# Optimization experiments

Measured on AMD Instinct MI355X. Metric: run time of the kernel, lower is better.

The kernel has to match this reference:

```python
import jax, jax.numpy as jnp
import numpy as np

N = 50000        # nodes
R = 51           # enriched relations (25 fwd + 25 inverse + self-loop)
F_IN = 32        # feat_size
E = 32           # embed_size
C = 16           # num_classes
B = 30           # num_bases
NNZ = 2_000_000  # nonzeros in vertical adjacency


def _xavier(key, shape):
    # mimics nn.init.xavier_uniform_ with gain for relu (sqrt(2))
    fan_in, fan_out = shape[-2], shape[-1]
    a = np.sqrt(2.0) * np.sqrt(6.0 / (fan_in + fan_out))
    return jax.random.uniform(key, shape, jnp.float32, -a, a)


def setup_inputs() -> dict:
    key = jax.random.key(0)
    ks = jax.random.split(key, 8)
    # COO of vertical adjacency, shape (R*N, N)
    rows = jax.random.randint(ks[0], (NNZ,), 0, R * N)
    cols = jax.random.randint(ks[1], (NNZ,), 0, N)
    # row-normalized values: vals = 1 / row_degree  (sum_sparse with rows=True)
    deg = jax.ops.segment_sum(jnp.ones((NNZ,), jnp.float32), rows, num_segments=R * N)
    vals = (1.0 / jnp.maximum(deg, 1.0))[rows]
    features = jax.random.normal(ks[2], (N, F_IN), jnp.float32)
    comps1 = _xavier(ks[3], (R, B))
    bases1 = _xavier(ks[4], (B, F_IN, E))
    comps2 = _xavier(ks[5], (R, B))
    bases2 = _xavier(ks[6], (B, E, C))
    bias1 = jnp.zeros((E,), jnp.float32)
    bias2 = jnp.zeros((C,), jnp.float32)
    return {
        "features": features, "vals": vals,
        "comps1": comps1, "bases1": bases1, "bias1": bias1,
        "comps2": comps2, "bases2": bases2, "bias2": bias2,
        "rows": rows, "cols": cols,
    }


def _spmm(rows, cols, vals, x):
    # (R*N, N) sparse @ (N, f) dense -> (R*N, f)
    return jax.ops.segment_sum(vals[:, None] * x[cols], rows, num_segments=R * N)


def reference(features, vals, comps1, bases1, bias1, comps2, bases2, bias2, rows, cols):
    # layer 1: SpMM then basis-decomposed per-relation mixing
    h = _spmm(rows, cols, vals, features).reshape(R, N, F_IN)   # (r, n, f)
    w1 = jnp.einsum('rb,bfe->rfe', comps1, bases1)              # (r, f, e)
    h = jnp.einsum('rnf,rfe->ne', h, w1)                        # (n, e)
    h = jax.nn.relu(h + bias1)
    # layer 2
    h = _spmm(rows, cols, vals, h).reshape(R, N, E)             # (r, n, e)
    w2 = jnp.einsum('rb,bho->rho', comps2, bases2)              # (r, e, c)
    h = jnp.einsum('rho,rnh->no', w2, h)                        # (n, c)
    return h + bias2
```

## Files before the change

kernel.cpp:

```cpp
#include <hip/hip_runtime.h>

#define NNODES 50000
#define RREL 51
#define FIN 32
#define EDIM 32
#define CDIM 16
#define BB 30
#define NNZ_ 2000000
#define CAP_ 2000896
#define EPB 4096
#define NBUK 391

typedef unsigned int uint32;
typedef unsigned short ushort;
typedef uint32 u32x2 __attribute__((ext_vector_type(2)));
typedef uint32 u32x4 __attribute__((ext_vector_type(4)));
typedef short bf16x8 __attribute__((ext_vector_type(8)));
typedef float f32x4 __attribute__((ext_vector_type(4)));

static __device__ __forceinline__ uint32 pack_bf16x2(float a, float b) {
    uint32 ua = __builtin_bit_cast(uint32, a);
    uint32 ub = __builtin_bit_cast(uint32, b);
    ua += 0x7fffu + ((ua >> 16) & 1u);
    ub += 0x7fffu + ((ub >> 16) & 1u);
    return (ua >> 16) | (ub & 0xffff0000u);
}
static __device__ __forceinline__ ushort bf16_1(float x) {
    uint32 u = __builtin_bit_cast(uint32, x);
    u += 0x7fffu + ((u >> 16) & 1u);
    return (ushort)(u >> 16);
}
static __device__ __forceinline__ float unpack_lo(uint32 u) { return __builtin_bit_cast(float, u << 16); }
static __device__ __forceinline__ float unpack_hi(uint32 u) { return __builtin_bit_cast(float, u & 0xffff0000u); }

__global__ void k_weights(const float* __restrict__ comps1, const float* __restrict__ bases1,
                          const float* __restrict__ comps2, const float* __restrict__ bases2,
                          ushort* __restrict__ Wb1, ushort* __restrict__ Wb2) {
    int i = blockIdx.x * 256 + threadIdx.x;
    if (i < RREL * FIN * EDIM) {
        int r = i >> 10, fe = i & 1023, f = fe >> 5, e = fe & 31;
        float acc = 0.f;
#pragma unroll
        for (int b = 0; b < BB; b++) acc += comps1[r * BB + b] * bases1[b * 1024 + fe];
        Wb1[((r * 4 + (f >> 3)) * 32 + e) * 8 + (f & 7)] = bf16_1(acc);
    }
    if (i < RREL * EDIM * CDIM) {
        int r = i >> 9, ec = i & 511, kk = ec >> 4, c = ec & 15;
        float acc = 0.f;
#pragma unroll
        for (int b = 0; b < BB; b++) acc += comps2[r * BB + b] * bases2[b * 512 + ec];
        Wb2[((r * 4 + (kk >> 3)) * 16 + c) * 8 + (kk & 7)] = bf16_1(acc);
    }
}

__global__ void k_tobf16(const float2* __restrict__ src, uint32* __restrict__ dst, int n2) {
    int i = blockIdx.x * 256 + threadIdx.x;
    if (i < n2) {
        float2 f = src[i];
        dst[i] = pack_bf16x2(f.x, f.y);
    }
}

__global__ __launch_bounds__(1024) void k_relhist(const int* __restrict__ rows,
                                                  int* __restrict__ rel_cnt) {
    __shared__ int lc[RREL];
    int t = threadIdx.x;
    if (t < RREL) lc[t] = 0;
    __syncthreads();
    size_t k = (size_t)blockIdx.x * EPB + (size_t)t * 4;
    int rr[4];
    if (k + 4 <= NNZ_) {
        int4 rw = *(const int4*)(rows + k);
        rr[0] = rw.x; rr[1] = rw.y; rr[2] = rw.z; rr[3] = rw.w;
    } else {
#pragma unroll
        for (int j = 0; j < 4; j++) rr[j] = (k + j < NNZ_) ? rows[k + j] : -1;
    }
#pragma unroll
    for (int j = 0; j < 4; j++)
        if (rr[j] >= 0) atomicAdd(&lc[rr[j] / NNODES], 1);
    __syncthreads();
    if (t < RREL) atomicAdd(&rel_cnt[t], lc[t]);
}

__global__ void k_relscan(const int* __restrict__ rel_cnt, int* __restrict__ pad_base,
                          int* __restrict__ rel_cur) {
    if (threadIdx.x == 0) {
        int a = 0;
        for (int r = 0; r < RREL; r++) {
            pad_base[r] = a; rel_cur[r] = a;
            a += (rel_cnt[r] + 15) & ~15;
        }
        pad_base[RREL] = a;
    }
}

__global__ void k_padfill(const int* __restrict__ rel_cnt, const int* __restrict__ pad_base,
                          int* __restrict__ s_pk, int* __restrict__ s_src,
                          float* __restrict__ s_val, int* __restrict__ buk_cnt) {
    int r = blockIdx.x;
    int start, end, relv;
    if (r < RREL) { start = pad_base[r] + rel_cnt[r]; end = pad_base[r + 1]; relv = r; }
    else { start = pad_base[RREL]; end = CAP_; relv = 0; }
    if (threadIdx.x == 0 && end > start) atomicAdd(&buk_cnt[NBUK - 1], end - start);
    int pkpad = (int)(((uint32)relv << 25) | (uint32)NNODES);
    for (int i = start + threadIdx.x; i < end; i += 64) {
        s_pk[i] = pkpad;
        s_src[i] = 0;
        s_val[i] = 0.f;
    }
}

__global__ __launch_bounds__(1024) void k_scatter(const int* __restrict__ rows, const int* __restrict__ cols,
                                                  const float* __restrict__ vals, int* __restrict__ rel_cur,
                                                  int* __restrict__ buk_cnt,
                                                  int* __restrict__ s_pk, int* __restrict__ s_src,
                                                  float* __restrict__ s_val) {
    __shared__ int lcnt[RREL], lbase[RREL], gbase[RREL];
    __shared__ int bukc[NBUK];
    __shared__ int stotal;
    __shared__ uint32 st[EPB];
    int t = threadIdx.x;
    size_t base = (size_t)blockIdx.x * EPB;
    if (t < RREL) lcnt[t] = 0;
    if (t < NBUK) bukc[t] = 0;
    __syncthreads();
    size_t k = base + (size_t)t * 4;
    int relv[4], dstv[4];
    {
        int rr[4];
        if (k + 4 <= NNZ_) {
            int4 rw = *(const int4*)(rows + k);
            rr[0] = rw.x; rr[1] = rw.y; rr[2] = rw.z; rr[3] = rw.w;
        } else {
#pragma unroll
            for (int j = 0; j < 4; j++) rr[j] = (k + j < NNZ_) ? rows[k + j] : -1;
        }
#pragma unroll
        for (int j = 0; j < 4; j++) {
            if (rr[j] >= 0) {
                int rel = rr[j] / NNODES;
                relv[j] = rel;
                dstv[j] = rr[j] - rel * NNODES;
                atomicAdd(&lcnt[rel], 1);
                atomicAdd(&bukc[dstv[j] >> 7], 1);
            } else relv[j] = -1;
        }
    }
    __syncthreads();
    if (t < 64) {
        int v = (t < RREL) ? lcnt[t] : 0;
        int sum = v;
#pragma unroll
        for (int off = 1; off < 64; off <<= 1) {
            int u = __shfl_up(sum, off, 64);
            if (t >= off) sum += u;
        }
        if (t < RREL) { lbase[t] = sum - v; gbase[t] = atomicAdd(&rel_cur[t], v); }
        if (t == RREL - 1) stotal = sum;
    }
    if (t < NBUK) atomicAdd(&buk_cnt[t], bukc[t]);
    __syncthreads();
    if (t < RREL) lcnt[t] = 0;
    __syncthreads();
#pragma unroll
    for (int j = 0; j < 4; j++) {
        int rel = relv[j];
        if (rel >= 0) {
            int slot = lbase[rel] + atomicAdd(&lcnt[rel], 1);
            st[slot] = ((uint32)dstv[j] << 12) | (uint32)(t * 4 + j);
        }
    }
    __syncthreads();
    int total = stotal;
#pragma unroll
    for (int i = 0; i < 4; i++) {
        int s2 = t + i * 1024;
        if (s2 < total) {
            uint32 u = st[s2];
            int dst = (int)(u >> 12);
            size_t orig = base + (u & 4095u);
            int rel = rows[orig] / NNODES;
            int g = gbase[rel] + (s2 - lbase[rel]);
            s_pk[g] = (int)(((uint32)rel << 25) | (uint32)dst);
            s_src[g] = cols[orig];
            s_val[g] = vals[orig];
        }
    }
}

__global__ void k_bukscan(const int* __restrict__ buk_cnt, int* __restrict__ buk_base,
                          int* __restrict__ buk_cur) {
    if (threadIdx.x == 0) {
        int a = 0;
        for (int b = 0; b < NBUK; b++) { buk_base[b] = a; buk_cur[b] = a; a += buk_cnt[b]; }
        buk_base[NBUK] = a;
    }
}

__global__ __launch_bounds__(1024) void k_bucket(const int* __restrict__ s_pk,
                                                 int* __restrict__ buk_cur,
                                                 u32x2* __restrict__ tok8) {
    __shared__ int bukc[NBUK], lbase2[NBUK], gbase2[NBUK];
    __shared__ int ssum[1024];
    __shared__ u32x2 st8[EPB];
    int t = threadIdx.x;
    size_t base = (size_t)blockIdx.x * EPB;
    int total = (int)(((size_t)CAP_ - base < (size_t)EPB) ? ((size_t)CAP_ - base) : (size_t)EPB);
    if (t < NBUK) bukc[t] = 0;
    __syncthreads();
    size_t k = base + (size_t)t * 4;
    int pkv[4], bv[4];
    if (k + 4 <= CAP_) {
        int4 q = *(const int4*)(s_pk + k);
        pkv[0] = q.x; pkv[1] = q.y; pkv[2] = q.z; pkv[3] = q.w;
#pragma unroll
        for (int j = 0; j < 4; j++) bv[j] = (int)(((uint32)pkv[j] & 0x1FFFFFFu) >> 7);
    } else {
#pragma unroll
        for (int j = 0; j < 4; j++) {
            if (k + j < CAP_) { pkv[j] = s_pk[k + j]; bv[j] = (int)(((uint32)pkv[j] & 0x1FFFFFFu) >> 7); }
            else bv[j] = -1;
        }
    }
#pragma unroll
    for (int j = 0; j < 4; j++)
        if (bv[j] >= 0) atomicAdd(&bukc[bv[j]], 1);
    __syncthreads();
    int v = (t < NBUK) ? bukc[t] : 0;
    ssum[t] = v;
    __syncthreads();
    for (int off = 1; off < 1024; off <<= 1) {
        int u = (t >= off) ? ssum[t - off] : 0;
        __syncthreads();
        ssum[t] += u;
        __syncthreads();
    }
    if (t < NBUK) { lbase2[t] = ssum[t] - v; gbase2[t] = atomicAdd(&buk_cur[t], v); }
    __syncthreads();
    if (t < NBUK) bukc[t] = 0;
    __syncthreads();
#pragma unroll
    for (int j = 0; j < 4; j++) {
        if (bv[j] >= 0) {
            int slot = lbase2[bv[j]] + atomicAdd(&bukc[bv[j]], 1);
            u32x2 w; w.x = (uint32)pkv[j]; w.y = (uint32)(k + j);
            st8[slot] = w;
        }
    }
    __syncthreads();
    for (int s2 = t; s2 < total; s2 += 1024) {
        u32x2 w = st8[s2];
        int b = (int)((w.x & 0x1FFFFFFu) >> 7);
        tok8[gbase2[b] + (s2 - lbase2[b])] = w;
    }
}

__global__ __launch_bounds__(256) void k_rank(const u32x2* __restrict__ tok8,
                                              const int* __restrict__ buk_base,
                                              int* __restrict__ dst_base,
                                              int* __restrict__ s_pk) {
    __shared__ int lcnt[128], lexc[128], lrank[128], ssc[128];
    int b = blockIdx.x, t = threadIdx.x;
    int lo = buk_base[b], hi = buk_base[b + 1];
    int d0 = b << 7;
    if (t < 128) lcnt[t] = 0;
    __syncthreads();
    for (int i = lo + t; i < hi; i += 256) {
        int dl = (int)(tok8[i].x & 0x1FFFFFFu) - d0;
        atomicAdd(&lcnt[dl], 1);
    }
    __syncthreads();
    int v = (t < 128) ? lcnt[t] : 0;
    if (t < 128) ssc[t] = v;
    __syncthreads();
    for (int off = 1; off < 128; off <<= 1) {
        int u = (t >= off && t < 128) ? ssc[t - off] : 0;
        __syncthreads();
        if (t < 128) ssc[t] += u;
        __syncthreads();
    }
    if (t < 128) {
        lexc[t] = ssc[t] - v;
        int d = d0 + t;
        if (d <= NNODES) dst_base[d] = lo + lexc[t];
        lrank[t] = 0;
    }
    __syncthreads();
    for (int i = lo + t; i < hi; i += 256) {
        u32x2 w = tok8[i];
        int dl = (int)(w.x & 0x1FFFFFFu) - d0;
        int q = lo + lexc[dl] + atomicAdd(&lrank[dl], 1);
        s_pk[(int)w.y] = (int)((w.x & 0xFE000000u) | (uint32)q);
    }
}

template <int FO>
__global__ __launch_bounds__(256) void k_edgeA(const int* __restrict__ s_pk,
                                               const int* __restrict__ s_src,
                                               const float* __restrict__ s_val,
                                               const u32x4* __restrict__ Xb,
                                               const u32x4* __restrict__ Wb,
                                               uint32* __restrict__ y) {
    const int NT = FO / 16;
    const int NW = (FO == 32) ? 32 : 16;
    int t = threadIdx.x, lane = t & 63, wv = t >> 6;
    int ln15 = lane & 15, quad = lane >> 4;
    size_t k0 = (size_t)blockIdx.x * 512 + wv * 128;

    int pk0 = s_pk[k0 + lane],  pk1 = s_pk[k0 + 64 + lane];
    int sc0 = s_src[k0 + lane], sc1 = s_src[k0 + 64 + lane];
    float v0 = s_val[k0 + lane], v1 = s_val[k0 + 64 + lane];

    f32x4 acc[8][NT];
    const f32x4 zero = {0.f, 0.f, 0.f, 0.f};
#pragma unroll
    for (int s = 0; s < 8; s++) {
        int osc = (s < 4) ? sc0 : sc1;
        int opk = (s < 4) ? pk0 : pk1;
        int srcs = __shfl(osc, (s & 3) * 16 + ln15, 64);
        int rels = (int)(((uint32)__builtin_amdgcn_readfirstlane(__shfl(opk, (s & 3) * 16, 64))) >> 25);
        bf16x8 a = __builtin_bit_cast(bf16x8, Xb[(size_t)srcs * 4 + quad]);
#pragma unroll
        for (int tt = 0; tt < NT; tt++) {
            bf16x8 b = __builtin_bit_cast(bf16x8, Wb[(rels * 4 + quad) * NW + ln15 + 16 * tt]);
            acc[s][tt] = __builtin_amdgcn_mfma_f32_16x16x32_bf16(a, b, zero, 0, 0, 0);
        }
    }

#pragma unroll
    for (int s = 0; s < 8; s++) {
        int opk = (s < 4) ? pk0 : pk1;
        float ov = (s < 4) ? v0 : v1;
#pragma unroll
        for (int rg = 0; rg < 4; rg++) {
            int e = (s & 3) * 16 + quad * 4 + rg;
            float ve = __shfl(ov, e, 64);
            int pe = __shfl(opk, e, 64) & 0x1FFFFFF;
            if (FO == 32) {
                uint32 val = pack_bf16x2(acc[s][0][rg] * ve, acc[s][1][rg] * ve);
                y[(size_t)pe * 16 + ln15] = val;
            } else {
                ((ushort*)y)[(size_t)pe * 16 + ln15] = bf16_1(acc[s][0][rg] * ve);
            }
        }
    }
}

template <int FO, bool RELU, bool BF16OUT>
__global__ __launch_bounds__(256) void k_segB(const uint32* __restrict__ y,
                                              const int* __restrict__ dst_base,
                                              const float* __restrict__ bias,
                                              void* __restrict__ outp) {
    const int UPR = FO / 2;
    const int QL = UPR / 4;
    const int RPI = 64 / QL;
    const bool ILV = (FO == 32);
    int t = threadIdx.x, lane = t & 63, wv = t >> 6;
    int dst = blockIdx.x * 4 + wv;
    if (dst >= NNODES) return;
    int s = dst_base[dst], e2 = dst_base[dst + 1];
    int q = lane % QL, r = lane / QL;
    float acc[8];
#pragma unroll
    for (int j = 0; j < 8; j++) acc[j] = 0.f;
    for (int i = s + r; i < e2; i += RPI) {
        u32x4 u = __builtin_nontemporal_load((const u32x4*)(y + (size_t)i * UPR + 4 * q));
        acc[0] += unpack_lo(u.x); acc[1] += unpack_hi(u.x);
        acc[2] += unpack_lo(u.y); acc[3] += unpack_hi(u.y);
        acc[4] += unpack_lo(u.z); acc[5] += unpack_hi(u.z);
        acc[6] += unpack_lo(u.w); acc[7] += unpack_hi(u.w);
    }
#pragma unroll
    for (int off = 32; off >= QL; off >>= 1)
#pragma unroll
        for (int j = 0; j < 8; j++) acc[j] += __shfl_down(acc[j], off, 64);
    if (lane < QL) {
        float o[8];
        if (ILV) {
#pragma unroll
            for (int j = 0; j < 4; j++) {
                o[2 * j]     = acc[2 * j]     + bias[4 * q + j];
                o[2 * j + 1] = acc[2 * j + 1] + bias[4 * q + 16 + j];
                if (RELU) { o[2 * j] = fmaxf(o[2 * j], 0.f); o[2 * j + 1] = fmaxf(o[2 * j + 1], 0.f); }
            }
        } else {
#pragma unroll
            for (int j = 0; j < 8; j++) {
                o[j] = acc[j] + bias[8 * q + j];
                if (RELU) o[j] = fmaxf(o[j], 0.f);
            }
        }
        if (BF16OUT) {
            if (ILV) {
                u32x2 a0, a1;
                a0.x = pack_bf16x2(o[0], o[2]); a0.y = pack_bf16x2(o[4], o[6]);
                a1.x = pack_bf16x2(o[1], o[3]); a1.y = pack_bf16x2(o[5], o[7]);
                ((u32x2*)outp)[(size_t)dst * 8 + q] = a0;
                ((u32x2*)outp)[(size_t)dst * 8 + 4 + q] = a1;
            } else {
                u32x4 pk;
                pk.x = pack_bf16x2(o[0], o[1]); pk.y = pack_bf16x2(o[2], o[3]);
                pk.z = pack_bf16x2(o[4], o[5]); pk.w = pack_bf16x2(o[6], o[7]);
                ((u32x4*)outp)[(size_t)dst * QL + q] = pk;
            }
        } else {
            float4* op = (float4*)outp;
            op[(size_t)dst * (FO / 4) + 2 * q]     = make_float4(o[0], o[1], o[2], o[3]);
            op[(size_t)dst * (FO / 4) + 2 * q + 1] = make_float4(o[4], o[5], o[6], o[7]);
        }
    }
}

extern "C" void kernel_launch(void* const* d_in, const int* in_sizes, int n_in,
                              void* d_out, int out_size, void* d_ws, size_t ws_size,
                              hipStream_t stream) {
    const float* features = (const float*)d_in[0];
    const float* vals     = (const float*)d_in[1];
    const float* comps1   = (const float*)d_in[2];
    const float* bases1   = (const float*)d_in[3];
    const float* bias1    = (const float*)d_in[4];
    const float* comps2   = (const float*)d_in[5];
    const float* bases2   = (const float*)d_in[6];
    const float* bias2    = (const float*)d_in[7];
    const int*   rows     = (const int*)d_in[8];
    const int*   cols     = (const int*)d_in[9];
    float* out = (float*)d_out;

    float* ws = (float*)d_ws;
    size_t o = 0;
    ushort* Wb1 = (ushort*)(ws + o); o += RREL * FIN * EDIM / 2;
    ushort* Wb2 = (ushort*)(ws + o); o += RREL * EDIM * CDIM / 2;
    o = (o + 3) & ~(size_t)3;
    uint32* Xb  = (uint32*)(ws + o); o += (size_t)NNODES * (FIN / 2);
    uint32* h1b = (uint32*)(ws + o); o += (size_t)NNODES * (EDIM / 2);
    int* s_pk  = (int*)(ws + o); o += CAP_;
    int* s_src = (int*)(ws + o); o += CAP_;
    float* s_val = ws + o;       o += CAP_;
    int* rel_cnt  = (int*)(ws + o); o += RREL + 1;
    int* buk_cnt  = (int*)(ws + o); o += NBUK + 1;
    int* rel_cur  = (int*)(ws + o); o += RREL;
    int* pad_base = (int*)(ws + o); o += RREL + 1;
    int* buk_base = (int*)(ws + o); o += NBUK + 1;
    int* buk_cur  = (int*)(ws + o); o += NBUK;
    o = (o + 3) & ~(size_t)3;
    int* dst_base = (int*)(ws + o); o += NNODES + 4;
    o = (o + 3) & ~(size_t)3;
    uint32* y = (uint32*)(ws + o);
    u32x2* tok8 = (u32x2*)y;

    const int NB = (NNZ_ + EPB - 1) / EPB;
    const int NB2 = (CAP_ + EPB - 1) / EPB;

    hipMemsetAsync(rel_cnt, 0, (RREL + 1 + NBUK + 1) * sizeof(int), stream);

    k_weights<<<(RREL * FIN * EDIM + 255) / 256, 256, 0, stream>>>(comps1, bases1, comps2, bases2, Wb1, Wb2);
    k_tobf16<<<(NNODES * FIN / 2 + 255) / 256, 256, 0, stream>>>((const float2*)features, Xb, NNODES * FIN / 2);
    k_relhist<<<NB, 1024, 0, stream>>>(rows, rel_cnt);
    k_relscan<<<1, 64, 0, stream>>>(rel_cnt, pad_base, rel_cur);
    k_padfill<<<RREL + 1, 64, 0, stream>>>(rel_cnt, pad_base, s_pk, s_src, s_val, buk_cnt);
    k_scatter<<<NB, 1024, 0, stream>>>(rows, cols, vals, rel_cur, buk_cnt, s_pk, s_src, s_val);
    k_bukscan<<<1, 64, 0, stream>>>(buk_cnt, buk_base, buk_cur);
    k_bucket<<<NB2, 1024, 0, stream>>>(s_pk, buk_cur, tok8);
    k_rank<<<NBUK, 256, 0, stream>>>(tok8, buk_base, dst_base, s_pk);

    k_edgeA<EDIM><<<CAP_ / 512, 256, 0, stream>>>(s_pk, s_src, s_val, (const u32x4*)Xb,
                                                  (const u32x4*)Wb1, y);
    k_segB<EDIM, true, true><<<(NNODES + 3) / 4, 256, 0, stream>>>(y, dst_base, bias1, h1b);
    k_edgeA<CDIM><<<CAP_ / 512, 256, 0, stream>>>(s_pk, s_src, s_val, (const u32x4*)h1b,
                                                  (const u32x4*)Wb2, y);
    k_segB<CDIM, false, false><<<(NNODES + 3) / 4, 256, 0, stream>>>(y, dst_base, bias2, out);
}
```

Measured before the change: 375.1 us.

## Replace relation-sorted edge pipeline with destination-sorted fused basis-space aggregation

Edges are now bucketed straight from the COO input by destination node, with each destination padded to a multiple of sixteen. This drops the relation scatter, the pad fill and the rank passes. A fused kernel per layer gathers neighbour features and mixes them into basis space using the comps coefficients held in shared memory. It then multiplies by the bases with MFMA and applies bias and relu, so the large per-edge intermediate y and the separate segment-sum kernel are no longer needed. This trades per-relation weight materialisation for a projection against 30 bases. It adds per-destination padding overhead and more complex shared-memory staging.

```diff
diff --git a/kernel.cpp b/kernel.cpp
--- a/kernel.cpp
+++ b/kernel.cpp
@@ -7,9 +7,9 @@
 #define CDIM 16
 #define BB 30
 #define NNZ_ 2000000
-#define CAP_ 2000896
 #define EPB 4096
 #define NBUK 391
+#define PCAP_MAX 2750128
 
 typedef unsigned int uint32;
 typedef unsigned short ushort;
@@ -17,6 +17,7 @@
 typedef uint32 u32x4 __attribute__((ext_vector_type(4)));
 typedef short bf16x8 __attribute__((ext_vector_type(8)));
 typedef float f32x4 __attribute__((ext_vector_type(4)));
+typedef float f32x16 __attribute__((ext_vector_type(16)));
 
 static __device__ __forceinline__ uint32 pack_bf16x2(float a, float b) {
     uint32 ua = __builtin_bit_cast(uint32, a);
@@ -30,26 +31,21 @@
     u += 0x7fffu + ((u >> 16) & 1u);
     return (ushort)(u >> 16);
 }
-static __device__ __forceinline__ float unpack_lo(uint32 u) { return __builtin_bit_cast(float, u << 16); }
-static __device__ __forceinline__ float unpack_hi(uint32 u) { return __builtin_bit_cast(float, u & 0xffff0000u); }
-
-__global__ void k_weights(const float* __restrict__ comps1, const float* __restrict__ bases1,
-                          const float* __restrict__ comps2, const float* __restrict__ bases2,
-                          ushort* __restrict__ Wb1, ushort* __restrict__ Wb2) {
+
+__global__ void k_weights2(const float* __restrict__ bases1, const float* __restrict__ bases2,
+                           ushort* __restrict__ Wb1, ushort* __restrict__ Wb2) {
     int i = blockIdx.x * 256 + threadIdx.x;
-    if (i < RREL * FIN * EDIM) {
-        int r = i >> 10, fe = i & 1023, f = fe >> 5, e = fe & 31;
-        float acc = 0.f;
-#pragma unroll
-        for (int b = 0; b < BB; b++) acc += comps1[r * BB + b] * bases1[b * 1024 + fe];
-        Wb1[((r * 4 + (f >> 3)) * 32 + e) * 8 + (f & 7)] = bf16_1(acc);
-    }
-    if (i < RREL * EDIM * CDIM) {
-        int r = i >> 9, ec = i & 511, kk = ec >> 4, c = ec & 15;
-        float acc = 0.f;
-#pragma unroll
-        for (int b = 0; b < BB; b++) acc += comps2[r * BB + b] * bases2[b * 512 + ec];
-        Wb2[((r * 4 + (kk >> 3)) * 16 + c) * 8 + (kk & 7)] = bf16_1(acc);
+    if (i < 960 * 32) {
+        int e = i & 31, k = i >> 5;
+        int b = k >> 5, f = k & 31;
+        float v = bases1[b * 1024 + f * 32 + e];
+        Wb1[((k >> 3) * 32 + e) * 8 + (k & 7)] = bf16_1(v);
+    }
+    if (i < 960 * 16) {
+        int e = i & 15, k = i >> 4;
+        int b = k >> 5, h = k & 31;
+        float v = bases2[b * 512 + h * 16 + e];
+        Wb2[((k >> 3) * 16 + e) * 8 + (k & 7)] = bf16_1(v);
     }
 }
 
@@ -61,11 +57,11 @@
     }
 }
 
-__global__ __launch_bounds__(1024) void k_relhist(const int* __restrict__ rows,
-                                                  int* __restrict__ rel_cnt) {
-    __shared__ int lc[RREL];
+__global__ __launch_bounds__(1024) void k_bukhist(const int* __restrict__ rows,
+                                                  int* __restrict__ buk_cnt) {
+    __shared__ int lc[NBUK];
     int t = threadIdx.x;
-    if (t < RREL) lc[t] = 0;
+    if (t < NBUK) lc[t] = 0;
     __syncthreads();
     size_t k = (size_t)blockIdx.x * EPB + (size_t)t * 4;
     int rr[4];
@@ -78,119 +74,17 @@
     }
 #pragma unroll
     for (int j = 0; j < 4; j++)
-        if (rr[j] >= 0) atomicAdd(&lc[rr[j] / NNODES], 1);
-    __syncthreads();
-    if (t < RREL) atomicAdd(&rel_cnt[t], lc[t]);
-}
-
-__global__ void k_relscan(const int* __restrict__ rel_cnt, int* __restrict__ pad_base,
-                          int* __restrict__ rel_cur) {
-    if (threadIdx.x == 0) {
-        int a = 0;
-        for (int r = 0; r < RREL; r++) {
-            pad_base[r] = a; rel_cur[r] = a;
-            a += (rel_cnt[r] + 15) & ~15;
-        }
-        pad_base[RREL] = a;
-    }
-}
-
-__global__ void k_padfill(const int* __restrict__ rel_cnt, const int* __restrict__ pad_base,
-                          int* __restrict__ s_pk, int* __restrict__ s_src,
-                          float* __restrict__ s_val, int* __restrict__ buk_cnt) {
-    int r = blockIdx.x;
-    int start, end, relv;
-    if (r < RREL) { start = pad_base[r] + rel_cnt[r]; end = pad_base[r + 1]; relv = r; }
-    else { start = pad_base[RREL]; end = CAP_; relv = 0; }
-    if (threadIdx.x == 0 && end > start) atomicAdd(&buk_cnt[NBUK - 1], end - start);
-    int pkpad = (int)(((uint32)relv << 25) | (uint32)NNODES);
-    for (int i = start + threadIdx.x; i < end; i += 64) {
-        s_pk[i] = pkpad;
-        s_src[i] = 0;
-        s_val[i] = 0.f;
-    }
-}
-
-__global__ __launch_bounds__(1024) void k_scatter(const int* __restrict__ rows, const int* __restrict__ cols,
-                                                  const float* __restrict__ vals, int* __restrict__ rel_cur,
-                                                  int* __restrict__ buk_cnt,
-                                                  int* __restrict__ s_pk, int* __restrict__ s_src,
-                                                  float* __restrict__ s_val) {
-    __shared__ int lcnt[RREL], lbase[RREL], gbase[RREL];
-    __shared__ int bukc[NBUK];
-    __shared__ int stotal;
-    __shared__ uint32 st[EPB];
-    int t = threadIdx.x;
-    size_t base = (size_t)blockIdx.x * EPB;
-    if (t < RREL) lcnt[t] = 0;
-    if (t < NBUK) bukc[t] = 0;
-    __syncthreads();
-    size_t k = base + (size_t)t * 4;
-    int relv[4], dstv[4];
-    {
-        int rr[4];
-        if (k + 4 <= NNZ_) {
-            int4 rw = *(const int4*)(rows + k);
-            rr[0] = rw.x; rr[1] = rw.y; rr[2] = rw.z; rr[3] = rw.w;
-        } else {
-#pragma unroll
-            for (int j = 0; j < 4; j++) rr[j] = (k + j < NNZ_) ? rows[k + j] : -1;
-        }
-#pragma unroll
-        for (int j = 0; j < 4; j++) {
-            if (rr[j] >= 0) {
-                int rel = rr[j] / NNODES;
-                relv[j] = rel;
-                dstv[j] = rr[j] - rel * NNODES;
-                atomicAdd(&lcnt[rel], 1);
-                atomicAdd(&bukc[dstv[j] >> 7], 1);
-            } else relv[j] = -1;
-        }
-    }
-    __syncthreads();
-    if (t < 64) {
-        int v = (t < RREL) ? lcnt[t] : 0;
-        int sum = v;
-#pragma unroll
-        for (int off = 1; off < 64; off <<= 1) {
-            int u = __shfl_up(sum, off, 64);
-            if (t >= off) sum += u;
-        }
-        if (t < RREL) { lbase[t] = sum - v; gbase[t] = atomicAdd(&rel_cur[t], v); }
-        if (t == RREL - 1) stotal = sum;
-    }
-    if (t < NBUK) atomicAdd(&buk_cnt[t], bukc[t]);
-    __syncthreads();
-    if (t < RREL) lcnt[t] = 0;
-    __syncthreads();
-#pragma unroll
-    for (int j = 0; j < 4; j++) {
-        int rel = relv[j];
-        if (rel >= 0) {
-            int slot = lbase[rel] + atomicAdd(&lcnt[rel], 1);
-            st[slot] = ((uint32)dstv[j] << 12) | (uint32)(t * 4 + j);
-        }
-    }
-    __syncthreads();
-    int total = stotal;
-#pragma unroll
-    for (int i = 0; i < 4; i++) {
-        int s2 = t + i * 1024;
-        if (s2 < total) {
-            uint32 u = st[s2];
-            int dst = (int)(u >> 12);
-            size_t orig = base + (u & 4095u);
-            int rel = rows[orig] / NNODES;
-            int g = gbase[rel] + (s2 - lbase[rel]);
-            s_pk[g] = (int)(((uint32)rel << 25) | (uint32)dst);
-            s_src[g] = cols[orig];
-            s_val[g] = vals[orig];
-        }
-    }
-}
-
-__global__ void k_bukscan(const int* __restrict__ buk_cnt, int* __restrict__ buk_base,
-                          int* __restrict__ buk_cur) {
+        if (rr[j] >= 0) {
+            int rel = rr[j] / NNODES;
+            int dst = rr[j] - rel * NNODES;
+            atomicAdd(&lc[dst >> 7], 1);
+        }
+    __syncthreads();
+    if (t < NBUK) atomicAdd(&buk_cnt[t], lc[t]);
+}
+
+__global__ void k_scan1(const int* __restrict__ buk_cnt, int* __restrict__ buk_base,
+                        int* __restrict__ buk_cur) {
     if (threadIdx.x == 0) {
         int a = 0;
         for (int b = 0; b < NBUK; b++) { buk_base[b] = a; buk_cur[b] = a; a += buk_cnt[b]; }
@@ -198,29 +92,50 @@
     }
 }
 
-__global__ __launch_bounds__(1024) void k_bucket(const int* __restrict__ s_pk,
-                                                 int* __restrict__ buk_cur,
-                                                 u32x2* __restrict__ tok8) {
-    __shared__ int bukc[NBUK], lbase2[NBUK], gbase2[NBUK];
+__global__ __launch_bounds__(1024) void k_bucket2(const int* __restrict__ rows,
+                                                  const int* __restrict__ cols,
+                                                  const float* __restrict__ vals,
+                                                  int* __restrict__ buk_cur,
+                                                  u32x2* __restrict__ tok8,
+                                                  float* __restrict__ sval_b) {
+    __shared__ int bukc[NBUK], lb[NBUK], gb[NBUK];
     __shared__ int ssum[1024];
     __shared__ u32x2 st8[EPB];
+    __shared__ float sv[EPB];
     int t = threadIdx.x;
     size_t base = (size_t)blockIdx.x * EPB;
-    int total = (int)(((size_t)CAP_ - base < (size_t)EPB) ? ((size_t)CAP_ - base) : (size_t)EPB);
+    int total = (int)(((size_t)NNZ_ - base < (size_t)EPB) ? ((size_t)NNZ_ - base) : (size_t)EPB);
     if (t < NBUK) bukc[t] = 0;
     __syncthreads();
     size_t k = base + (size_t)t * 4;
-    int pkv[4], bv[4];
-    if (k + 4 <= CAP_) {
-        int4 q = *(const int4*)(s_pk + k);
-        pkv[0] = q.x; pkv[1] = q.y; pkv[2] = q.z; pkv[3] = q.w;
-#pragma unroll
-        for (int j = 0; j < 4; j++) bv[j] = (int)(((uint32)pkv[j] & 0x1FFFFFFu) >> 7);
+    int bv[4]; uint32 tx[4], ty[4]; float vv[4];
+    if (k + 4 <= NNZ_) {
+        int4 rw = *(const int4*)(rows + k);
+        int4 cw = *(const int4*)(cols + k);
+        float4 vw = *(const float4*)(vals + k);
+        int rr[4] = {rw.x, rw.y, rw.z, rw.w};
+        int cc[4] = {cw.x, cw.y, cw.z, cw.w};
+        vv[0] = vw.x; vv[1] = vw.y; vv[2] = vw.z; vv[3] = vw.w;
+#pragma unroll
+        for (int j = 0; j < 4; j++) {
+            int rel = rr[j] / NNODES;
+            int dst = rr[j] - rel * NNODES;
+            bv[j] = dst >> 7;
+            tx[j] = (uint32)dst | ((uint32)rel << 16);
+            ty[j] = (uint32)cc[j] | ((uint32)rel << 16);
+        }
     } else {
 #pragma unroll
         for (int j = 0; j < 4; j++) {
-            if (k + j < CAP_) { pkv[j] = s_pk[k + j]; bv[j] = (int)(((uint32)pkv[j] & 0x1FFFFFFu) >> 7); }
-            else bv[j] = -1;
+            if (k + j < NNZ_) {
+                int r = rows[k + j];
+                int rel = r / NNODES;
+                int dst = r - rel * NNODES;
+                bv[j] = dst >> 7;
+                tx[j] = (uint32)dst | ((uint32)rel << 16);
+                ty[j] = (uint32)cols[k + j] | ((uint32)rel << 16);
+                vv[j] = vals[k + j];
+            } else bv[j] = -1;
         }
     }
 #pragma unroll
@@ -236,43 +151,70 @@
         ssum[t] += u;
         __syncthreads();
     }
-    if (t < NBUK) { lbase2[t] = ssum[t] - v; gbase2[t] = atomicAdd(&buk_cur[t], v); }
+    if (t < NBUK) { lb[t] = ssum[t] - v; gb[t] = atomicAdd(&buk_cur[t], v); }
     __syncthreads();
     if (t < NBUK) bukc[t] = 0;
     __syncthreads();
 #pragma unroll
     for (int j = 0; j < 4; j++) {
         if (bv[j] >= 0) {
-            int slot = lbase2[bv[j]] + atomicAdd(&bukc[bv[j]], 1);
-            u32x2 w; w.x = (uint32)pkv[j]; w.y = (uint32)(k + j);
+            int slot = lb[bv[j]] + atomicAdd(&bukc[bv[j]], 1);
+            u32x2 w; w.x = tx[j]; w.y = ty[j];
             st8[slot] = w;
-        }
-    }
-    __syncthreads();
-    for (int s2 = t; s2 < total; s2 += 1024) {
-        u32x2 w = st8[s2];
-        int b = (int)((w.x & 0x1FFFFFFu) >> 7);
-        tok8[gbase2[b] + (s2 - lbase2[b])] = w;
-    }
-}
-
-__global__ __launch_bounds__(256) void k_rank(const u32x2* __restrict__ tok8,
-                                              const int* __restrict__ buk_base,
-                                              int* __restrict__ dst_base,
-                                              int* __restrict__ s_pk) {
+            sv[slot] = vv[j];
+        }
+    }
+    __syncthreads();
+    for (int s = t; s < total; s += 1024) {
+        u32x2 w = st8[s];
+        int bk = (int)((w.x & 0xFFFFu) >> 7);
+        int pos = gb[bk] + (s - lb[bk]);
+        tok8[pos] = w;
+        sval_b[pos] = sv[s];
+    }
+}
+
+__global__ __launch_bounds__(256) void k_rank3a(const u32x2* __restrict__ tok8,
+                                                const int* __restrict__ buk_base,
+                                                int* __restrict__ pbuk_cnt) {
+    __shared__ int lcnt[128];
+    __shared__ int tot;
+    int b = blockIdx.x, t = threadIdx.x;
+    if (t < 128) lcnt[t] = 0;
+    if (t == 0) tot = 0;
+    __syncthreads();
+    int lo = buk_base[b], hi = buk_base[b + 1];
+    for (int i = lo + t; i < hi; i += 256) atomicAdd(&lcnt[tok8[i].x & 127], 1);
+    __syncthreads();
+    if (t < 128) atomicAdd(&tot, (lcnt[t] + 15) & ~15);
+    __syncthreads();
+    if (t == 0) pbuk_cnt[b] = tot;
+}
+
+__global__ void k_scan2(const int* __restrict__ pbuk_cnt, int* __restrict__ pbuk_base) {
+    if (threadIdx.x == 0) {
+        int a = 0;
+        for (int b = 0; b < NBUK; b++) { pbuk_base[b] = a; a += pbuk_cnt[b]; }
+        pbuk_base[NBUK] = a;
+    }
+}
+
+__global__ __launch_bounds__(256) void k_place(const u32x2* __restrict__ tok8,
+                                               const float* __restrict__ sval_b,
+                                               const int* __restrict__ buk_base,
+                                               const int* __restrict__ pbuk_base,
+                                               int* __restrict__ pdst_base,
+                                               uint32* __restrict__ pe_sr,
+                                               float* __restrict__ pe_val) {
     __shared__ int lcnt[128], lexc[128], lrank[128], ssc[128];
     int b = blockIdx.x, t = threadIdx.x;
-    int lo = buk_base[b], hi = buk_base[b + 1];
-    int d0 = b << 7;
-    if (t < 128) lcnt[t] = 0;
-    __syncthreads();
-    for (int i = lo + t; i < hi; i += 256) {
-        int dl = (int)(tok8[i].x & 0x1FFFFFFu) - d0;
-        atomicAdd(&lcnt[dl], 1);
-    }
-    __syncthreads();
-    int v = (t < 128) ? lcnt[t] : 0;
-    if (t < 128) ssc[t] = v;
+    int lo = buk_base[b], hi = buk_base[b + 1], pb = pbuk_base[b];
+    if (t < 128) { lcnt[t] = 0; lrank[t] = 0; }
+    __syncthreads();
+    for (int i = lo + t; i < hi; i += 256) atomicAdd(&lcnt[tok8[i].x & 127], 1);
+    __syncthreads();
+    int v = 0;
+    if (t < 128) { v = (lcnt[t] + 15) & ~15; ssc[t] = v; }
     __syncthreads();
     for (int off = 1; off < 128; off <<= 1) {
         int u = (t >= off && t < 128) ? ssc[t - off] : 0;
@@ -282,132 +224,142 @@
     }
     if (t < 128) {
         lexc[t] = ssc[t] - v;
-        int d = d0 + t;
-        if (d <= NNODES) dst_base[d] = lo + lexc[t];
-        lrank[t] = 0;
+        int d = (b << 7) + t;
+        if (d <= NNODES) pdst_base[d] = pb + lexc[t];
     }
     __syncthreads();
     for (int i = lo + t; i < hi; i += 256) {
         u32x2 w = tok8[i];
-        int dl = (int)(w.x & 0x1FFFFFFu) - d0;
-        int q = lo + lexc[dl] + atomicAdd(&lrank[dl], 1);
-        s_pk[(int)w.y] = (int)((w.x & 0xFE000000u) | (uint32)q);
-    }
-}
-
-template <int FO>
-__global__ __launch_bounds__(256) void k_edgeA(const int* __restrict__ s_pk,
-                                               const int* __restrict__ s_src,
-                                               const float* __restrict__ s_val,
+        int dl = (int)(w.x & 127u);
+        int pos = pb + lexc[dl] + atomicAdd(&lrank[dl], 1);
+        pe_sr[pos] = w.y;
+        pe_val[pos] = sval_b[i];
+    }
+    if (t < 128) {
+        int s0 = pb + lexc[t] + lcnt[t];
+        int s1 = pb + lexc[t] + ((lcnt[t] + 15) & ~15);
+        for (int i = s0; i < s1; i++) { pe_sr[i] = 0u; pe_val[i] = 0.f; }
+    }
+}
+
+template <int FO, bool RELU, bool BF16OUT>
+__global__ __launch_bounds__(256) void k_fused(const uint32* __restrict__ pe_sr,
+                                               const float* __restrict__ pe_val,
+                                               const int* __restrict__ pdst_base,
                                                const u32x4* __restrict__ Xb,
                                                const u32x4* __restrict__ Wb,
-                                               uint32* __restrict__ y) {
-    const int NT = FO / 16;
-    const int NW = (FO == 32) ? 32 : 16;
+                                               const float* __restrict__ comps,
+                                               const float* __restrict__ bias,
+                                               void* __restrict__ outp) {
+    __shared__ float comps_l[RREL * 32];
+    __shared__ uint32 eds[4][64];
+    __shared__ float edv[4][64];
+    __shared__ __align__(16) ushort xst[4][4][512];
+    __shared__ __align__(16) ushort ubuf[4][4][968];
     int t = threadIdx.x, lane = t & 63, wv = t >> 6;
+    for (int i = t; i < RREL * 32; i += 256) {
+        int r = i >> 5, b = i & 31;
+        comps_l[i] = (b < BB) ? comps[r * BB + b] : 0.f;
+    }
+    __syncthreads();
+    int m = lane & 31, hf = lane >> 5, k0 = hf * 8;
     int ln15 = lane & 15, quad = lane >> 4;
-    size_t k0 = (size_t)blockIdx.x * 512 + wv * 128;
-
-    int pk0 = s_pk[k0 + lane],  pk1 = s_pk[k0 + 64 + lane];
-    int sc0 = s_src[k0 + lane], sc1 = s_src[k0 + 64 + lane];
-    float v0 = s_val[k0 + lane], v1 = s_val[k0 + 64 + lane];
-
-    f32x4 acc[8][NT];
-    const f32x4 zero = {0.f, 0.f, 0.f, 0.f};
-#pragma unroll
-    for (int s = 0; s < 8; s++) {
-        int osc = (s < 4) ? sc0 : sc1;
-        int opk = (s < 4) ? pk0 : pk1;
-        int srcs = __shfl(osc, (s & 3) * 16 + ln15, 64);
-        int rels = (int)(((uint32)__builtin_amdgcn_readfirstlane(__shfl(opk, (s & 3) * 16, 64))) >> 25);
-        bf16x8 a = __builtin_bit_cast(bf16x8, Xb[(size_t)srcs * 4 + quad]);
-#pragma unroll
-        for (int tt = 0; tt < NT; tt++) {
-            bf16x8 b = __builtin_bit_cast(bf16x8, Wb[(rels * 4 + quad) * NW + ln15 + 16 * tt]);
-            acc[s][tt] = __builtin_amdgcn_mfma_f32_16x16x32_bf16(a, b, zero, 0, 0, 0);
-        }
-    }
-
-#pragma unroll
-    for (int s = 0; s < 8; s++) {
-        int opk = (s < 4) ? pk0 : pk1;
-        float ov = (s < 4) ? v0 : v1;
-#pragma unroll
-        for (int rg = 0; rg < 4; rg++) {
-            int e = (s & 3) * 16 + quad * 4 + rg;
-            float ve = __shfl(ov, e, 64);
-            int pe = __shfl(opk, e, 64) & 0x1FFFFFF;
-            if (FO == 32) {
-                uint32 val = pack_bf16x2(acc[s][0][rg] * ve, acc[s][1][rg] * ve);
-                y[(size_t)pe * 16 + ln15] = val;
-            } else {
-                ((ushort*)y)[(size_t)pe * 16 + ln15] = bf16_1(acc[s][0][rg] * ve);
+    int d0 = (blockIdx.x * 4 + wv) * 8;
+#pragma unroll 1
+    for (int batch = 0; batch < 2; batch++) {
+        int db = d0 + batch * 4;
+#pragma unroll 1
+        for (int s = 0; s < 4; s++) {
+            int d = db + s;
+            if (d >= NNODES) break;
+            int lo = pdst_base[d], segEnd = pdst_base[d + 1];
+            f32x16 acc;
+#pragma unroll
+            for (int i = 0; i < 16; i++) acc[i] = 0.f;
+#pragma unroll 1
+            for (int c0 = lo; c0 < segEnd; c0 += 64) {
+                eds[wv][lane] = pe_sr[c0 + lane];
+                edv[wv][lane] = pe_val[c0 + lane];
+                int nwin = (segEnd - c0) >> 4;
+                if (nwin > 4) nwin = 4;
+#pragma unroll 1
+                for (int wi = 0; wi < nwin; wi++) {
+                    int src = (int)(eds[wv][wi * 16 + (lane >> 2)] & 0xFFFFu);
+                    u32x4 xv = Xb[(size_t)src * 4 + (lane & 3)];
+                    *(u32x4*)&xst[wv][wi][lane * 8] = xv;
+                }
+#pragma unroll 1
+                for (int wi = 0; wi < nwin; wi++) {
+                    const ushort* xs = &xst[wv][wi][0];
+                    uint32 bw0, bw1, bw2, bw3;
+                    {
+                        uint32 a0 = xs[(k0 + 0) * 32 + m], a1 = xs[(k0 + 1) * 32 + m];
+                        uint32 a2 = xs[(k0 + 2) * 32 + m], a3 = xs[(k0 + 3) * 32 + m];
+                        uint32 a4 = xs[(k0 + 4) * 32 + m], a5 = xs[(k0 + 5) * 32 + m];
+                        uint32 a6 = xs[(k0 + 6) * 32 + m], a7 = xs[(k0 + 7) * 32 + m];
+                        bw0 = a0 | (a1 << 16); bw1 = a2 | (a3 << 16);
+                        bw2 = a4 | (a5 << 16); bw3 = a6 | (a7 << 16);
+                    }
+                    u32x4 bvq = { bw0, bw1, bw2, bw3 };
+                    float cc[8];
+#pragma unroll
+                    for (int j = 0; j < 8; j++) {
+                        uint32 sr = eds[wv][wi * 16 + k0 + j];
+                        float vv = edv[wv][wi * 16 + k0 + j];
+                        cc[j] = vv * comps_l[((sr >> 16) << 5) | m];
+                    }
+                    u32x4 avq = { pack_bf16x2(cc[0], cc[1]), pack_bf16x2(cc[2], cc[3]),
+                                  pack_bf16x2(cc[4], cc[5]), pack_bf16x2(cc[6], cc[7]) };
+                    acc = __builtin_amdgcn_mfma_f32_32x32x16_bf16(
+                        __builtin_bit_cast(bf16x8, avq), __builtin_bit_cast(bf16x8, bvq),
+                        acc, 0, 0, 0);
+                }
             }
-        }
-    }
-}
-
-template <int FO, bool RELU, bool BF16OUT>
-__global__ __launch_bounds__(256) void k_segB(const uint32* __restrict__ y,
-                                              const int* __restrict__ dst_base,
-                                              const float* __restrict__ bias,
-                                              void* __restrict__ outp) {
-    const int UPR = FO / 2;
-    const int QL = UPR / 4;
-    const int RPI = 64 / QL;
-    const bool ILV = (FO == 32);
-    int t = threadIdx.x, lane = t & 63, wv = t >> 6;
-    int dst = blockIdx.x * 4 + wv;
-    if (dst >= NNODES) return;
-    int s = dst_base[dst], e2 = dst_base[dst + 1];
-    int q = lane % QL, r = lane / QL;
-    float acc[8];
-#pragma unroll
-    for (int j = 0; j < 8; j++) acc[j] = 0.f;
-    for (int i = s + r; i < e2; i += RPI) {
-        u32x4 u = __builtin_nontemporal_load((const u32x4*)(y + (size_t)i * UPR + 4 * q));
-        acc[0] += unpack_lo(u.x); acc[1] += unpack_hi(u.x);
-        acc[2] += unpack_lo(u.y); acc[3] += unpack_hi(u.y);
-        acc[4] += unpack_lo(u.z); acc[5] += unpack_hi(u.z);
-        acc[6] += unpack_lo(u.w); acc[7] += unpack_hi(u.w);
-    }
-#pragma unroll
-    for (int off = 32; off >= QL; off >>= 1)
-#pragma unroll
-        for (int j = 0; j < 8; j++) acc[j] += __shfl_down(acc[j], off, 64);
-    if (lane < QL) {
-        float o[8];
-        if (ILV) {
-#pragma unroll
-            for (int j = 0; j < 4; j++) {
-                o[2 * j]     = acc[2 * j]     + bias[4 * q + j];
-                o[2 * j + 1] = acc[2 * j + 1] + bias[4 * q + 16 + j];
-                if (RELU) { o[2 * j] = fmaxf(o[2 * j], 0.f); o[2 * j + 1] = fmaxf(o[2 * j + 1], 0.f); }
+#pragma unroll
+            for (int r = 0; r < 16; r++) {
+                int b = (r & 3) + 8 * (r >> 2) + 4 * hf;
+                float vme = acc[r];
+                float vot = __shfl_xor(vme, 1, 64);
+                if (b < BB && !(m & 1)) {
+                    *(uint32*)&ubuf[wv][s][b * 32 + m] = pack_bf16x2(vme, vot);
+                }
             }
-        } else {
-#pragma unroll
-            for (int j = 0; j < 8; j++) {
-                o[j] = acc[j] + bias[8 * q + j];
-                if (RELU) o[j] = fmaxf(o[j], 0.f);
+        }
+        const int NT = FO / 16;
+        f32x4 acc2[NT];
+#pragma unroll
+        for (int tt = 0; tt < NT; tt++)
+#pragma unroll
+            for (int i = 0; i < 4; i++) acc2[tt][i] = 0.f;
+#pragma unroll 6
+        for (int ks = 0; ks < 30; ks++) {
+            bf16x8 af = *(const bf16x8*)&ubuf[wv][ln15 & 3][ks * 32 + quad * 8];
+#pragma unroll
+            for (int tt = 0; tt < NT; tt++) {
+                bf16x8 bf2 = __builtin_bit_cast(bf16x8, Wb[(ks * 4 + quad) * FO + ln15 + 16 * tt]);
+                acc2[tt] = __builtin_amdgcn_mfma_f32_16x16x32_bf16(af, bf2, acc2[tt], 0, 0, 0);
             }
         }
-        if (BF16OUT) {
-            if (ILV) {
-                u32x2 a0, a1;
-                a0.x = pack_bf16x2(o[0], o[2]); a0.y = pack_bf16x2(o[4], o[6]);
-                a1.x = pack_bf16x2(o[1], o[3]); a1.y = pack_bf16x2(o[5], o[7]);
-                ((u32x2*)outp)[(size_t)dst * 8 + q] = a0;
-                ((u32x2*)outp)[(size_t)dst * 8 + 4 + q] = a1;
-            } else {
-                u32x4 pk;
-                pk.x = pack_bf16x2(o[0], o[1]); pk.y = pack_bf16x2(o[2], o[3]);
-                pk.z = pack_bf16x2(o[4], o[5]); pk.w = pack_bf16x2(o[6], o[7]);
-                ((u32x4*)outp)[(size_t)dst * QL + q] = pk;
+        if (quad == 0) {
+#pragma unroll
+            for (int r = 0; r < 4; r++) {
+                int dst = db + r;
+                if (dst < NNODES) {
+                    if (BF16OUT) {
+                        ushort* hp = (ushort*)outp;
+#pragma unroll
+                        for (int tt = 0; tt < NT; tt++) {
+                            float o = acc2[tt][r] + bias[ln15 + 16 * tt];
+                            if (RELU) o = fmaxf(o, 0.f);
+                            hp[(size_t)dst * FO + ln15 + 16 * tt] = bf16_1(o);
+                        }
+                    } else {
+                        float o = acc2[0][r] + bias[ln15];
+                        if (RELU) o = fmaxf(o, 0.f);
+                        ((float*)outp)[(size_t)dst * FO + ln15] = o;
+                    }
+                }
             }
-        } else {
-            float4* op = (float4*)outp;
-            op[(size_t)dst * (FO / 4) + 2 * q]     = make_float4(o[0], o[1], o[2], o[3]);
-            op[(size_t)dst * (FO / 4) + 2 * q + 1] = make_float4(o[4], o[5], o[6], o[7]);
         }
     }
 }
@@ -429,45 +381,38 @@
 
     float* ws = (float*)d_ws;
     size_t o = 0;
-    ushort* Wb1 = (ushort*)(ws + o); o += RREL * FIN * EDIM / 2;
-    ushort* Wb2 = (ushort*)(ws + o); o += RREL * EDIM * CDIM / 2;
+    ushort* Wb1 = (ushort*)(ws + o); o += 960 * 32 / 2;
+    ushort* Wb2 = (ushort*)(ws + o); o += 960 * 16 / 2;
+    uint32* Xb  = (uint32*)(ws + o); o += (size_t)NNODES * 16;
+    uint32* h1b = (uint32*)(ws + o); o += (size_t)NNODES * 16;
+    uint32* pe_sr  = (uint32*)(ws + o); o += PCAP_MAX;
+    float*  pe_val = (float*)(ws + o);  o += PCAP_MAX;
+    int* pdst_base = (int*)(ws + o); o += NNODES + 8;
+    int* buk_cnt   = (int*)(ws + o); o += NBUK;
+    int* buk_base  = (int*)(ws + o); o += NBUK + 1;
+    int* buk_cur   = (int*)(ws + o); o += NBUK;
+    int* pbuk_cnt  = (int*)(ws + o); o += NBUK;
+    int* pbuk_base = (int*)(ws + o); o += NBUK + 1;
     o = (o + 3) & ~(size_t)3;
-    uint32* Xb  = (uint32*)(ws + o); o += (size_t)NNODES * (FIN / 2);
-    uint32* h1b = (uint32*)(ws + o); o += (size_t)NNODES * (EDIM / 2);
-    int* s_pk  = (int*)(ws + o); o += CAP_;
-    int* s_src = (int*)(ws + o); o += CAP_;
-    float* s_val = ws + o;       o += CAP_;
-    int* rel_cnt  = (int*)(ws + o); o += RREL + 1;
-    int* buk_cnt  = (int*)(ws + o); o += NBUK + 1;
-    int* rel_cur  = (int*)(ws + o); o += RREL;
-    int* pad_base = (int*)(ws + o); o += RREL + 1;
-    int* buk_base = (int*)(ws + o); o += NBUK + 1;
-    int* buk_cur  = (int*)(ws + o); o += NBUK;
-    o = (o + 3) & ~(size_t)3;
-    int* dst_base = (int*)(ws + o); o += NNODES + 4;
-    o = (o + 3) & ~(size_t)3;
-    uint32* y = (uint32*)(ws + o);
-    u32x2* tok8 = (u32x2*)y;
+    u32x2* tok8 = (u32x2*)(ws + o); o += 2 * (size_t)NNZ_;
+    float* sval_b = (float*)(ws + o); o += (size_t)NNZ_;
 
     const int NB = (NNZ_ + EPB - 1) / EPB;
-    const int NB2 = (CAP_ + EPB - 1) / EPB;
-
-    hipMemsetAsync(rel_cnt, 0, (RREL + 1 + NBUK + 1) * sizeof(int), stream);
-
-    k_weights<<<(RREL * FIN * EDIM + 255) / 256, 256, 0, stream>>>(comps1, bases1, comps2, bases2, Wb1, Wb2);
-    k_tobf16<<<(NNODES * FIN / 2 + 255) / 256, 256, 0, stream>>>((const float2*)features, Xb, NNODES * FIN / 2);
-    k_relhist<<<NB, 1024, 0, stream>>>(rows, rel_cnt);
-    k_relscan<<<1, 64, 0, stream>>>(rel_cnt, pad_base, rel_cur);
-    k_padfill<<<RREL + 1, 64, 0, stream>>>(rel_cnt, pad_base, s_pk, s_src, s_val, buk_cnt);
-    k_scatter<<<NB, 1024, 0, stream>>>(rows, cols, vals, rel_cur, buk_cnt, s_pk, s_src, s_val);
-    k_bukscan<<<1, 64, 0, stream>>>(buk_cnt, buk_base, buk_cur);
-    k_bucket<<<NB2, 1024, 0, stream>>>(s_pk, buk_cur, tok8);
-    k_rank<<<NBUK, 256, 0, stream>>>(tok8, buk_base, dst_base, s_pk);
-
-    k_edgeA<EDIM><<<CAP_ / 512, 256, 0, stream>>>(s_pk, s_src, s_val, (const u32x4*)Xb,
-                                                  (const u32x4*)Wb1, y);
-    k_segB<EDIM, true, true><<<(NNODES + 3) / 4, 256, 0, stream>>>(y, dst_base, bias1, h1b);
-    k_edgeA<CDIM><<<CAP_ / 512, 256, 0, stream>>>(s_pk, s_src, s_val, (const u32x4*)h1b,
-                                                  (const u32x4*)Wb2, y);
-    k_segB<CDIM, false, false><<<(NNODES + 3) / 4, 256, 0, stream>>>(y, dst_base, bias2, out);
-}
+
+    hipMemsetAsync(buk_cnt, 0, NBUK * sizeof(int), stream);
+
+    k_weights2<<<(960 * 32 + 255) / 256, 256, 0, stream>>>(bases1, bases2, Wb1, Wb2);
+    k_tobf16<<<(NNODES * FIN / 2 + 255) / 256, 256, 0, stream>>>((const float2*)features, Xb,
+                                                                 NNODES * FIN / 2);
+    k_bukhist<<<NB, 1024, 0, stream>>>(rows, buk_cnt);
+    k_scan1<<<1, 64, 0, stream>>>(buk_cnt, buk_base, buk_cur);
+    k_bucket2<<<NB, 1024, 0, stream>>>(rows, cols, vals, buk_cur, tok8, sval_b);
+    k_rank3a<<<NBUK, 256, 0, stream>>>(tok8, buk_base, pbuk_cnt);
+    k_scan2<<<1, 64, 0, stream>>>(pbuk_cnt, pbuk_base);
+    k_place<<<NBUK, 256, 0, stream>>>(tok8, sval_b, buk_base, pbuk_base, pdst_base, pe_sr, pe_val);
+
+    k_fused<EDIM, true, true><<<(NNODES + 31) / 32, 256, 0, stream>>>(
+        pe_sr, pe_val, pdst_base, (const u32x4*)Xb, (const u32x4*)Wb1, comps1, bias1, h1b);
+    k_fused<CDIM, false, false><<<(NNODES + 31) / 32, 256, 0, stream>>>(
+        pe_sr, pe_val, pdst_base, (const u32x4*)h1b, (const u32x4*)Wb2, comps2, bias2, out);
+}
```

After: 439.5 us. 17.2% more time.
